# Kernel tuning notes

Hardware: AMD Instinct MI355X
Metric: run time of the kernel (lower is better)

The kernel has to match this reference:

```python
import jax, jax.numpy as jnp
import numpy as np

HIDDEN_DIM = 256
N = 8192


def setup_inputs() -> dict:
    key = jax.random.key(0)
    k1, k2, k3, k4 = jax.random.split(key, 4)
    img = jax.random.normal(k1, (N, HIDDEN_DIM), dtype=jnp.float32)
    text = jax.random.normal(k2, (N, HIDDEN_DIM), dtype=jnp.float32)
    # nn.Linear(hidden_dim, hidden_dim, bias=False) weights, shape [out, in]
    scale = 1.0 / np.sqrt(HIDDEN_DIM)
    Wq = jax.random.uniform(k3, (HIDDEN_DIM, HIDDEN_DIM), dtype=jnp.float32, minval=-scale, maxval=scale)
    Wk = jax.random.uniform(k4, (HIDDEN_DIM, HIDDEN_DIM), dtype=jnp.float32, minval=-scale, maxval=scale)
    return {"img": img, "text": text, "Wq": Wq, "Wk": Wk}


def reference(img, text, Wq, Wk):
    d = img.shape[-1]
    norm_fact = 1.0 / jnp.sqrt(jnp.asarray(d, dtype=img.dtype))
    Q = img @ Wq.T                       # [N, D]
    K = text @ Wk.T                      # [N, D]
    scores = Q @ K.T                     # [N, N]
    # softmax over dim=1 (keys), then scaled by 1/sqrt(D)
    attn = jax.nn.softmax(scores, axis=1) * norm_fact
    out_img = attn @ img                 # [N, D]
    out_text = attn @ text               # [N, D]
    return (out_img, out_text)
```

## Files before the change

### kernel.cpp

```cpp
#include <hip/hip_runtime.h>

typedef unsigned short ushort_t;
typedef unsigned int uint_t;
typedef __attribute__((ext_vector_type(8))) short short8;
typedef __attribute__((ext_vector_type(8))) _Float16 half8;
typedef __attribute__((ext_vector_type(4))) _Float16 half4;
typedef __attribute__((ext_vector_type(4))) float float4v;

#define MFMA_BF16(a, b, c) __builtin_amdgcn_mfma_f32_16x16x32_bf16((a), (b), (c), 0, 0, 0)
#define MFMA_F16(a, b, c) __builtin_amdgcn_mfma_f32_16x16x32_f16((a), (b), (c), 0, 0, 0)

#define NQ 8192
#define DIM 256
#define DV 512

__device__ __forceinline__ ushort_t f2bf(float x) {
  union { float f; uint_t u; } v; v.f = x;
  return (ushort_t)((v.u + 0x7fffu + ((v.u >> 16) & 1u)) >> 16);
}
__device__ __forceinline__ float bf2f(ushort_t b) {
  union { uint_t u; float f; } v; v.u = ((uint_t)b) << 16;
  return v.f;
}

__device__ __forceinline__ half8 cvt8h(const float* p) {
  float4v a = *(const float4v*)p;
  float4v b = *(const float4v*)(p + 4);
  half8 r;
  r[0] = (_Float16)a[0]; r[1] = (_Float16)a[1];
  r[2] = (_Float16)a[2]; r[3] = (_Float16)a[3];
  r[4] = (_Float16)b[0]; r[5] = (_Float16)b[1];
  r[6] = (_Float16)b[2]; r[7] = (_Float16)b[3];
  return r;
}

__device__ __forceinline__ half8 as_h8(short8 s) {
  union { short8 s; half8 h; } u; u.s = s; return u.h;
}

__device__ __forceinline__ void load_lds_16(const void* g, void* l) {
  __builtin_amdgcn_global_load_lds(
      (const __attribute__((address_space(1))) uint_t*)g,
      (__attribute__((address_space(3))) uint_t*)l, 16, 0, 0);
}

__device__ __forceinline__ void barrier_vm0_lgkm0() {
  asm volatile("s_waitcnt vmcnt(0) lgkmcnt(0)\ns_barrier" ::: "memory");
}
__device__ __forceinline__ void barrier_lgkm0() {
  asm volatile("s_waitcnt lgkmcnt(0)\ns_barrier" ::: "memory");
}

__global__ __launch_bounds__(256, 2) void pre_kernel(
    const float* __restrict__ img, const float* __restrict__ text,
    const float* __restrict__ Wq, const float* __restrict__ Wk,
    _Float16* __restrict__ Qh, _Float16* __restrict__ Kh,
    ushort_t* __restrict__ Vt) {
  __shared__ float tile[64][65];
  const int bid = blockIdx.x;
  const int tid = threadIdx.x;
  if (bid < 1024) {
    const int bx = bid & 127;
    const int by = (bid >> 7) & 3;
    const int bz = bid >> 9;
    const int lane = tid & 63;
    const int wv = tid >> 6;
    const int l16 = lane & 15;
    const int quad = lane >> 4;
    const float* A = bz ? text : img;
    const float* W = bz ? Wk : Wq;
    _Float16* C = bz ? Kh : Qh;
    const int row = bx * 64 + wv * 16 + l16;
    const int colbase = by * 64;

    float4v acc[4];
#pragma unroll
    for (int c = 0; c < 4; ++c) acc[c] = (float4v){0.f, 0.f, 0.f, 0.f};
#pragma unroll
    for (int f = 0; f < 8; ++f) {
      const int k0 = f * 32 + quad * 8;
      half8 af = cvt8h(A + (size_t)row * DIM + k0);
#pragma unroll
      for (int c = 0; c < 4; ++c) {
        half8 bfr = cvt8h(W + (size_t)(colbase + c * 16 + l16) * DIM + k0);
        acc[c] = MFMA_F16(af, bfr, acc[c]);
      }
    }
    const int rbase = bx * 64 + wv * 16 + quad * 4;
#pragma unroll
    for (int c = 0; c < 4; ++c)
#pragma unroll
      for (int r = 0; r < 4; ++r)
        C[(size_t)(rbase + r) * DIM + colbase + c * 16 + l16] = (_Float16)acc[c][r];
  } else {
    const int vb = bid - 1024;
    const int n0 = (vb & 127) * 64;
    const int c0 = (vb >> 7) * 64;
    const float* src = (c0 < 256) ? img : text;
    const int cc0 = (c0 < 256) ? c0 : (c0 - 256);
#pragma unroll
    for (int i = 0; i < 4; ++i) {
      const int r = i * 16 + (tid >> 4);
      const int c = (tid & 15) * 4;
      *(float4v*)&tile[r][c] = *(const float4v*)(src + (size_t)(n0 + r) * DIM + cc0 + c);
    }
    __syncthreads();
    const int c = tid >> 2;
    const int seg = tid & 3;
    ushort_t tmp[16];
#pragma unroll
    for (int t = 0; t < 16; ++t) tmp[t] = f2bf(tile[seg * 16 + t][c]);
    ushort_t* dst = Vt + (size_t)(c0 + c) * NQ + n0 + seg * 16;
    *(short8*)dst = *(short8*)&tmp[0];
    *(short8*)(dst + 8) = *(short8*)&tmp[8];
  }
}

__device__ __forceinline__ void stage_K(const _Float16* __restrict__ Kh, int k0,
                                        ushort_t* dst, int tid, int wv) {
#pragma unroll
  for (int i = 0; i < 4; ++i) {
    const int chunk = i * 256 + tid;
    const int n = chunk >> 5;
    const int cs = (chunk & 31) ^ (n & 7);
    load_lds_16(Kh + (size_t)(k0 + n) * DIM + cs * 8,
                (char*)dst + (i * 256 + wv * 64) * 16);
  }
}
__device__ __forceinline__ void stage_V(const ushort_t* __restrict__ Vt, int k0,
                                        ushort_t* dst, int tid, int wv) {
#pragma unroll
  for (int i = 0; i < 8; ++i) {
    const int chunk = i * 256 + tid;
    const int vrow = chunk >> 2;
    const int dc = (chunk & 3) ^ ((vrow >> 1) & 3);
    load_lds_16(Vt + (size_t)vrow * NQ + k0 + dc * 8,
                (char*)dst + (i * 256 + wv * 64) * 16);
  }
}

__global__ __launch_bounds__(256, 2) void attn_kernel(
    const _Float16* __restrict__ Qh, const _Float16* __restrict__ Kh,
    const ushort_t* __restrict__ Vt, _Float16* __restrict__ pacc,
    float* __restrict__ pdenom, int kps, int ks) {
  extern __shared__ __align__(16) ushort_t smem[];
  ushort_t* ldsV = smem + 16384;

  const int tid = threadIdx.x;
  const int lane = tid & 63;
  const int wv = tid >> 6;
  const int l16 = lane & 15;
  const int quad = lane >> 4;
  const int id = blockIdx.x;
  const int split = id & (ks - 1);
  const int qtile = id / ks;
  const int kbeg = split * kps;
  const int sw2 = (l16 >> 1) & 3;
  const int swk = l16 & 7;

  short8 qf[8];
  {
    const _Float16* qptr = Qh + (size_t)(qtile * 64 + wv * 16 + l16) * DIM;
#pragma unroll
    for (int f = 0; f < 8; ++f)
      qf[f] = *(const short8*)(qptr + f * 32 + quad * 8);
  }

  float4v acc[4][8];
#pragma unroll
  for (int m = 0; m < 4; ++m)
#pragma unroll
    for (int c = 0; c < 8; ++c) acc[m][c] = (float4v){0.f, 0.f, 0.f, 0.f};
  float dacc[4] = {0.f, 0.f, 0.f, 0.f};

  const int ntiles = kps >> 5;

  stage_K(Kh, kbeg, smem, tid, wv);
  stage_V(Vt, kbeg, ldsV, tid, wv);

  for (int t = 0; t < ntiles; ++t) {
    const ushort_t* Kt = smem + (t & 1) * 8192;
    barrier_vm0_lgkm0();
    if (t + 1 < ntiles)
      stage_K(Kh, kbeg + (t + 1) * 32, smem + ((t + 1) & 1) * 8192, tid, wv);

    if (t > 0) {
      const ushort_t* Pprev = smem + 32768 + ((t - 1) & 1) * 2048;
      short8 pa[4];
#pragma unroll
      for (int m = 0; m < 4; ++m)
        pa[m] = *(const short8*)(Pprev + (m * 16 + l16) * 32 + (quad ^ sw2) * 8);
#pragma unroll
      for (int c = 0; c < 8; ++c) {
        const int vcol = (wv * 8 + c) * 16 + l16;
        short8 vb = *(const short8*)(ldsV + vcol * 32 + (quad ^ sw2) * 8);
#pragma unroll
        for (int m = 0; m < 4; ++m)
          acc[m][c] = MFMA_BF16(pa[m], vb, acc[m][c]);
      }
    }

    float4v s0 = (float4v){0.f, 0.f, 0.f, 0.f};
    float4v s1 = (float4v){0.f, 0.f, 0.f, 0.f};
#pragma unroll
    for (int f = 0; f < 8; ++f) {
      const int cs = ((f * 4 + quad) ^ swk) * 8;
      short8 kb0 = *(const short8*)(Kt + l16 * DIM + cs);
      short8 kb1 = *(const short8*)(Kt + (l16 + 16) * DIM + cs);
      s0 = MFMA_F16(as_h8(qf[f]), as_h8(kb0), s0);
      s1 = MFMA_F16(as_h8(qf[f]), as_h8(kb1), s1);
    }

    barrier_lgkm0();
    if (t >= 1) stage_V(Vt, kbeg + t * 32, ldsV, tid, wv);

    ushort_t* Pcur = smem + 32768 + (t & 1) * 2048;
    ushort_t pb0[4], pb1[4];
#pragma unroll
    for (int r = 0; r < 4; ++r) {
      pb0[r] = f2bf(__expf(s0[r]));
      pb1[r] = f2bf(__expf(s1[r]));
    }
#pragma unroll
    for (int r = 0; r < 4; ++r) {
      const int rb = wv * 16 + quad * 4 + r;
      const int swp = (rb >> 1) & 3;
      Pcur[rb * 32 + ((l16 >> 3) ^ swp) * 8 + (l16 & 7)] = pb0[r];
      Pcur[rb * 32 + ((2 + (l16 >> 3)) ^ swp) * 8 + (l16 & 7)] = pb1[r];
      dacc[r] += bf2f(pb0[r]) + bf2f(pb1[r]);
    }
  }

  barrier_vm0_lgkm0();
  {
    const ushort_t* Pprev = smem + 32768 + ((ntiles - 1) & 1) * 2048;
    short8 pa[4];
#pragma unroll
    for (int m = 0; m < 4; ++m)
      pa[m] = *(const short8*)(Pprev + (m * 16 + l16) * 32 + (quad ^ sw2) * 8);
#pragma unroll
    for (int c = 0; c < 8; ++c) {
      const int vcol = (wv * 8 + c) * 16 + l16;
      short8 vb = *(const short8*)(ldsV + vcol * 32 + (quad ^ sw2) * 8);
#pragma unroll
      for (int m = 0; m < 4; ++m)
        acc[m][c] = MFMA_BF16(pa[m], vb, acc[m][c]);
    }
  }

#pragma unroll
  for (int r = 0; r < 4; ++r) {
    float ts = dacc[r];
    ts += __shfl_xor(ts, 1);
    ts += __shfl_xor(ts, 2);
    ts += __shfl_xor(ts, 4);
    ts += __shfl_xor(ts, 8);
    dacc[r] = ts;
  }

  barrier_lgkm0();
  float* ldsD = (float*)smem;
  if (l16 == 0) {
#pragma unroll
    for (int r = 0; r < 4; ++r)
      ldsD[wv * 16 + quad * 4 + r] = dacc[r];
  }
  barrier_lgkm0();

  _Float16* pout = pacc + (size_t)split * ((size_t)NQ * DV);
#pragma unroll
  for (int m = 0; m < 4; ++m) {
    float invd[4];
#pragma unroll
    for (int r = 0; r < 4; ++r) invd[r] = 1.0f / ldsD[m * 16 + quad * 4 + r];
    const int rowbase = qtile * 64 + m * 16 + quad * 4;
#pragma unroll
    for (int c = 0; c < 8; ++c) {
      const int col = (wv * 8 + c) * 16 + l16;
#pragma unroll
      for (int r = 0; r < 4; ++r)
        pout[(size_t)(rowbase + r) * DV + col] = (_Float16)(acc[m][c][r] * invd[r]);
    }
  }
  if (l16 == 0) {
    const int rowbase = qtile * 64 + wv * 16 + quad * 4;
#pragma unroll
    for (int r = 0; r < 4; ++r)
      pdenom[split * NQ + rowbase + r] = dacc[r];
  }
}

__global__ __launch_bounds__(256) void combine_kernel(
    const _Float16* __restrict__ pacc, const float* __restrict__ pdenom,
    float* __restrict__ out, int ks) {
  const int idx = blockIdx.x * 256 + threadIdx.x;
  const int n = idx >> 6;
  const int c8 = (idx & 63) << 3;
  float s[8] = {0.f, 0.f, 0.f, 0.f, 0.f, 0.f, 0.f, 0.f};
  float dsum = 0.f;
  for (int sp = 0; sp < ks; ++sp) {
    const float d = pdenom[sp * NQ + n];
    half8 x = *(const half8*)(pacc + (size_t)sp * ((size_t)NQ * DV) + (size_t)n * DV + c8);
#pragma unroll
    for (int j = 0; j < 8; ++j) s[j] += d * (float)x[j];
    dsum += d;
  }
  const float scale = 1.0f / (16.0f * dsum);
  float4v lo = (float4v){s[0], s[1], s[2], s[3]} * scale;
  float4v hi = (float4v){s[4], s[5], s[6], s[7]} * scale;
  float* dst = (c8 < 256) ? (out + (size_t)n * DIM + c8)
                          : (out + (size_t)NQ * DIM + (size_t)n * DIM + (c8 - 256));
  *(float4v*)dst = lo;
  *(float4v*)(dst + 4) = hi;
}

extern "C" void kernel_launch(void* const* d_in, const int* in_sizes, int n_in,
                              void* d_out, int out_size, void* d_ws, size_t ws_size,
                              hipStream_t stream) {
  const float* img = (const float*)d_in[0];
  const float* text = (const float*)d_in[1];
  const float* Wq = (const float*)d_in[2];
  const float* Wk = (const float*)d_in[3];
  float* out = (float*)d_out;
  char* ws = (char*)d_ws;

  _Float16* Qh = (_Float16*)ws;
  _Float16* Kh = (_Float16*)(ws + ((size_t)4 << 20));
  ushort_t* Vt = (ushort_t*)(ws + ((size_t)8 << 20));
  const size_t accsz = (size_t)NQ * DV * sizeof(_Float16);
  const size_t base = (size_t)16 << 20;

  int ks = 4;
  if (ws_size < base + 4 * (accsz + NQ * sizeof(float))) ks = 2;
  _Float16* pacc = (_Float16*)(ws + base);
  float* pdenom = (float*)(ws + base + (size_t)ks * accsz);

  hipLaunchKernelGGL(pre_kernel, dim3(2048), dim3(256), 0, stream,
                     img, text, Wq, Wk, Qh, Kh, Vt);
  hipLaunchKernelGGL(attn_kernel, dim3(128 * ks), dim3(256),
                     36864 * sizeof(ushort_t), stream,
                     Qh, Kh, Vt, pacc, pdenom, NQ / ks, ks);
  hipLaunchKernelGGL(combine_kernel, dim3((NQ * DV / 8) / 256), dim3(256), 0, stream,
                     pacc, pdenom, out, ks);
}
```

Before: 244.7 us.

## Fuse split-K combine into attention kernel via last-block atomic counter

Removes the separate combine kernel launch. Each attention block atomically increments a per-query-tile counter, and the last split block to finish reduces the partial accumulators and denominators and writes the final output. Counters are zeroed in the pre kernel. This saves one launch and its tail, but the combine work is now serialized in one block per tile and adds a threadfence and atomic per block.

```diff
diff --git a/kernel.cpp b/kernel.cpp
--- a/kernel.cpp
+++ b/kernel.cpp
@@ -55,10 +55,11 @@
     const float* __restrict__ img, const float* __restrict__ text,
     const float* __restrict__ Wq, const float* __restrict__ Wk,
     _Float16* __restrict__ Qh, _Float16* __restrict__ Kh,
-    ushort_t* __restrict__ Vt) {
+    ushort_t* __restrict__ Vt, int* __restrict__ cnt) {
   __shared__ float tile[64][65];
   const int bid = blockIdx.x;
   const int tid = threadIdx.x;
+  if (bid == 0 && tid < 128) cnt[tid] = 0;
   if (bid < 1024) {
     const int bx = bid & 127;
     const int by = (bid >> 7) & 3;
@@ -142,7 +143,8 @@
 __global__ __launch_bounds__(256, 2) void attn_kernel(
     const _Float16* __restrict__ Qh, const _Float16* __restrict__ Kh,
     const ushort_t* __restrict__ Vt, _Float16* __restrict__ pacc,
-    float* __restrict__ pdenom, int kps, int ks) {
+    float* __restrict__ pdenom, int* __restrict__ cnt,
+    float* __restrict__ out, int kps, int ks) {
   extern __shared__ __align__(16) ushort_t smem[];
   ushort_t* ldsV = smem + 16384;
 
@@ -288,30 +290,42 @@
     for (int r = 0; r < 4; ++r)
       pdenom[split * NQ + rowbase + r] = dacc[r];
   }
-}
-
-__global__ __launch_bounds__(256) void combine_kernel(
-    const _Float16* __restrict__ pacc, const float* __restrict__ pdenom,
-    float* __restrict__ out, int ks) {
-  const int idx = blockIdx.x * 256 + threadIdx.x;
-  const int n = idx >> 6;
-  const int c8 = (idx & 63) << 3;
-  float s[8] = {0.f, 0.f, 0.f, 0.f, 0.f, 0.f, 0.f, 0.f};
-  float dsum = 0.f;
-  for (int sp = 0; sp < ks; ++sp) {
-    const float d = pdenom[sp * NQ + n];
-    half8 x = *(const half8*)(pacc + (size_t)sp * ((size_t)NQ * DV) + (size_t)n * DV + c8);
-#pragma unroll
-    for (int j = 0; j < 8; ++j) s[j] += d * (float)x[j];
-    dsum += d;
-  }
-  const float scale = 1.0f / (16.0f * dsum);
-  float4v lo = (float4v){s[0], s[1], s[2], s[3]} * scale;
-  float4v hi = (float4v){s[4], s[5], s[6], s[7]} * scale;
-  float* dst = (c8 < 256) ? (out + (size_t)n * DIM + c8)
-                          : (out + (size_t)NQ * DIM + (size_t)n * DIM + (c8 - 256));
-  *(float4v*)dst = lo;
-  *(float4v*)(dst + 4) = hi;
+
+  __threadfence();
+  __syncthreads();
+  int* lf = (int*)(smem + 128);
+  if (tid == 0) {
+    const int old = atomicAdd(&cnt[qtile], 1);
+    *lf = (old == ks - 1) ? 1 : 0;
+  }
+  __syncthreads();
+  if (*lf) {
+    __threadfence();
+    const int rowb = qtile * 64;
+#pragma unroll 2
+    for (int j = 0; j < 16; ++j) {
+      const int chunk = j * 256 + tid;
+      const int n = rowb + (chunk >> 6);
+      const int c8 = (chunk & 63) << 3;
+      float s[8] = {0.f, 0.f, 0.f, 0.f, 0.f, 0.f, 0.f, 0.f};
+      float dsum = 0.f;
+      for (int sp = 0; sp < ks; ++sp) {
+        const float d = pdenom[sp * NQ + n];
+        half8 x = *(const half8*)(pacc + (size_t)sp * ((size_t)NQ * DV) +
+                                  (size_t)n * DV + c8);
+#pragma unroll
+        for (int q = 0; q < 8; ++q) s[q] += d * (float)x[q];
+        dsum += d;
+      }
+      const float scale = 1.0f / (16.0f * dsum);
+      float4v lo = (float4v){s[0], s[1], s[2], s[3]} * scale;
+      float4v hi = (float4v){s[4], s[5], s[6], s[7]} * scale;
+      float* dst = (c8 < 256) ? (out + (size_t)n * DIM + c8)
+                              : (out + (size_t)NQ * DIM + (size_t)n * DIM + (c8 - 256));
+      *(float4v*)dst = lo;
+      *(float4v*)(dst + 4) = hi;
+    }
+  }
 }
 
 extern "C" void kernel_launch(void* const* d_in, const int* in_sizes, int n_in,
@@ -331,15 +345,14 @@
   const size_t base = (size_t)16 << 20;
 
   int ks = 4;
-  if (ws_size < base + 4 * (accsz + NQ * sizeof(float))) ks = 2;
+  if (ws_size < base + 4 * (accsz + NQ * sizeof(float)) + 1024) ks = 2;
   _Float16* pacc = (_Float16*)(ws + base);
   float* pdenom = (float*)(ws + base + (size_t)ks * accsz);
+  int* cnt = (int*)(ws + base + (size_t)ks * accsz + (size_t)ks * NQ * sizeof(float));
 
   hipLaunchKernelGGL(pre_kernel, dim3(2048), dim3(256), 0, stream,
-                     img, text, Wq, Wk, Qh, Kh, Vt);
+                     img, text, Wq, Wk, Qh, Kh, Vt, cnt);
   hipLaunchKernelGGL(attn_kernel, dim3(128 * ks), dim3(256),
                      36864 * sizeof(ushort_t), stream,
-                     Qh, Kh, Vt, pacc, pdenom, NQ / ks, ks);
-  hipLaunchKernelGGL(combine_kernel, dim3((NQ * DV / 8) / 256), dim3(256), 0, stream,
-                     pacc, pdenom, out, ks);
-}
+                     Qh, Kh, Vt, pacc, pdenom, cnt, out, NQ / ks, ks);
+}
```

Result: slower. 370.0 us (+51.2%).
